# Kernel tuning notes

Measured on AMD Instinct MI355X. Metric: run time of the kernel, lower is better.

The kernel has to match this reference:

```python
import jax, jax.numpy as jnp
import numpy as np

SPATIAL_SHAPES = ((100, 100), (50, 50), (25, 25), (13, 13))
B, C, NH, NL, NP, DFF = 4, 256, 8, 4, 4, 1024
HD = C // NH
L = sum(h * w for h, w in SPATIAL_SHAPES)  # 13294


def _xavier(key, shape):
    s = (6.0 / (shape[0] + shape[1])) ** 0.5
    return jax.random.uniform(key, shape, jnp.float32, -s, s)


def setup_inputs():
    key = jax.random.key(0)
    ks = jax.random.split(key, 12)
    ss = jnp.array(SPATIAL_SHAPES, jnp.int32)
    lsi = jnp.concatenate([jnp.zeros((1,), jnp.int32), jnp.cumsum(ss[:, 0] * ss[:, 1])[:-1].astype(jnp.int32)])
    return {
        "query": jax.random.normal(ks[0], (B, L, C), jnp.float32),
        "query_pos": jax.random.normal(ks[1], (B, L, C), jnp.float32),
        "reference_points": jax.random.uniform(ks[2], (B, L, NL, 2), jnp.float32),
        "spatial_shapes": ss,
        "level_start_index": lsi,
        "v_W": _xavier(ks[3], (C, C)), "v_b": jnp.zeros((C,), jnp.float32),
        "off_W": 0.01 * jax.random.normal(ks[4], (C, NH * NL * NP * 2), jnp.float32),
        "off_b": 0.1 * jax.random.normal(ks[5], (NH * NL * NP * 2,), jnp.float32),
        "aw_W": 0.01 * jax.random.normal(ks[6], (C, NH * NL * NP), jnp.float32),
        "aw_b": jnp.zeros((NH * NL * NP,), jnp.float32),
        "out_W": _xavier(ks[7], (C, C)), "out_b": jnp.zeros((C,), jnp.float32),
        "ln1_g": jnp.ones((C,), jnp.float32), "ln1_b": jnp.zeros((C,), jnp.float32),
        "lin1_W": _xavier(ks[8], (C, DFF)), "lin1_b": jnp.zeros((DFF,), jnp.float32),
        "lin2_W": _xavier(ks[9], (DFF, C)), "lin2_b": jnp.zeros((C,), jnp.float32),
        "ln2_g": jnp.ones((C,), jnp.float32), "ln2_b": jnp.zeros((C,), jnp.float32),
    }


def _layer_norm(x, g, b):
    mu = x.mean(-1, keepdims=True)
    var = ((x - mu) ** 2).mean(-1, keepdims=True)
    return (x - mu) * jax.lax.rsqrt(var + 1e-5) * g + b


def _msda(q, value, reference_points, v_W, v_b, off_W, off_b, aw_W, aw_b, out_W, out_b):
    # value projection, split heads -> [B, NH, L, HD]
    v = (value @ v_W + v_b).reshape(B, L, NH, HD).transpose(0, 2, 1, 3)
    off = (q @ off_W + off_b).reshape(B, L, NH, NL, NP, 2)
    aw = jax.nn.softmax((q @ aw_W + aw_b).reshape(B, L, NH, NL * NP), axis=-1)
    aw = aw.reshape(B, L, NH, NL, NP).transpose(0, 2, 1, 3, 4)  # [B,NH,L,NL,NP]
    # offset normalizer is (W, H) per level, matching (x, y) coords
    norm = jnp.array([[w, h] for h, w in SPATIAL_SHAPES], q.dtype)
    loc = reference_points[:, :, None, :, None, :] + off / norm[None, None, None, :, None, :]
    loc = loc.transpose(0, 2, 1, 3, 4, 5)  # [B,NH,L,NL,NP,2]
    acc = jnp.zeros((B, NH, L, HD), q.dtype)
    start = 0
    for l, (H_, W_) in enumerate(SPATIAL_SHAPES):
        v_l = jax.lax.dynamic_slice_in_dim(v, start, H_ * W_, axis=2)  # [B,NH,HW,HD]
        # grid_sample(align_corners=False): pixel = loc*size - 0.5
        x = loc[:, :, :, l, :, 0] * W_ - 0.5  # [B,NH,L,NP]
        y = loc[:, :, :, l, :, 1] * H_ - 0.5
        x0 = jnp.floor(x); y0 = jnp.floor(y)
        lx = x - x0; ly = y - y0
        x0i = x0.astype(jnp.int32); y0i = y0.astype(jnp.int32)

        def corner(yi, xi, w):
            valid = (yi >= 0) & (yi < H_) & (xi >= 0) & (xi < W_)  # zero padding
            idx = jnp.clip(yi, 0, H_ - 1) * W_ + jnp.clip(xi, 0, W_ - 1)
            g = jnp.take_along_axis(v_l, idx.reshape(B, NH, L * NP, 1), axis=2)
            g = g.reshape(B, NH, L, NP, HD)
            return g * (w * valid)[..., None]

        s = (corner(y0i, x0i, (1 - ly) * (1 - lx))
             + corner(y0i, x0i + 1, (1 - ly) * lx)
             + corner(y0i + 1, x0i, ly * (1 - lx))
             + corner(y0i + 1, x0i + 1, ly * lx))  # [B,NH,L,NP,HD]
        acc = acc + (s * aw[:, :, :, l, :, None]).sum(3)
        start += H_ * W_
    out = acc.transpose(0, 2, 1, 3).reshape(B, L, C)
    return out @ out_W + out_b


def _forward(query, query_pos, reference_points, v_W, v_b, off_W, off_b, aw_W, aw_b,
             out_W, out_b, ln1_g, ln1_b, lin1_W, lin1_b, lin2_W, lin2_b, ln2_g, ln2_b):
    q = query + query_pos
    src2 = _msda(q, query, reference_points, v_W, v_b, off_W, off_b, aw_W, aw_b, out_W, out_b)
    x = _layer_norm(query + src2, ln1_g, ln1_b)
    ffn = jax.nn.relu(x @ lin1_W + lin1_b) @ lin2_W + lin2_b
    return _layer_norm(x + ffn, ln2_g, ln2_b)


def reference(query, query_pos, reference_points, spatial_shapes, level_start_index,
              v_W, v_b, off_W, off_b, aw_W, aw_b, out_W, out_b,
              ln1_g, ln1_b, lin1_W, lin1_b, lin2_W, lin2_b, ln2_g, ln2_b):
    # spatial_shapes / level_start_index are consistent with the static SPATIAL_SHAPES
    # constant (shapes must be static for reshapes under jit).
    return _forward(query, query_pos, reference_points, v_W, v_b, off_W, off_b, aw_W, aw_b,
                    out_W, out_b, ln1_g, ln1_b, lin1_W, lin1_b, lin2_W, lin2_b, ln2_g, ln2_b)
```

## Files before the change

### kernel.cpp

```cpp
#include <hip/hip_runtime.h>
#include <hip/hip_bf16.h>
#include <cstddef>

constexpr int Ll   = 13294;
constexpr int NROW = 4 * Ll;
constexpr int MP   = 53248;

typedef __bf16       bf8v __attribute__((ext_vector_type(8)));
typedef __bf16       bf2v __attribute__((ext_vector_type(2)));
typedef float        f4v  __attribute__((ext_vector_type(4)));
typedef unsigned int u4v  __attribute__((ext_vector_type(4)));

#if defined(__has_builtin)
#  if __has_builtin(__builtin_amdgcn_fdot2_f32_bf16)
#    define HAVE_DOT2_BF16 1
#  endif
#endif
#ifndef HAVE_DOT2_BF16
#  define HAVE_DOT2_BF16 0
#endif

__device__ __forceinline__ void xcd_remap(int& m0, int& n0)
{
    const int nwg  = gridDim.x * gridDim.y;
    const int flat = blockIdx.y * gridDim.x + blockIdx.x;
    const int w    = (flat & 7) * (nwg >> 3) + (flat >> 3);
    n0 = (w % gridDim.x) * 128;
    m0 = (w / gridDim.x) * 128;
}

template<bool RELU, bool OUTF, bool OUTB>
__device__ __forceinline__
void gemm_body(const __hip_bfloat16* __restrict__ A, const __hip_bfloat16* __restrict__ Bt,
               const float* __restrict__ bias, const float* __restrict__ bias2,
               float* __restrict__ Cf, __hip_bfloat16* __restrict__ Cb,
               int N, int K, int m0, int n0,
               __hip_bfloat16 (*As)[128 * 32], __hip_bfloat16 (*Bs)[128 * 32])
{
    const int tid  = threadIdx.x;
    const int wid  = tid >> 6;
    const int lane = tid & 63;
    const int wm = wid >> 1, wn = wid & 1;
    const int fr = lane & 15, fq = lane >> 4;
    const int sr = lane >> 2;
    const int sc = (lane & 3) * 8;

    f4v acc[4][4] = {};

    for (int k0 = 0; k0 < K; k0 += 64) {
        #pragma unroll
        for (int h = 0; h < 2; ++h) {
            #pragma unroll
            for (int i = 0; i < 2; ++i) {
                const int s = wid * 2 + i;
                const __hip_bfloat16* sa = A  + (size_t)(m0 + s * 16 + sr) * K + k0 + h * 32 + sc;
                const __hip_bfloat16* sb = Bt + (size_t)(n0 + s * 16 + sr) * K + k0 + h * 32 + sc;
                __builtin_amdgcn_global_load_lds(
                    (const __attribute__((address_space(1))) void*)sa,
                    (__attribute__((address_space(3))) void*)&As[h][s * 512], 16, 0, 0);
                __builtin_amdgcn_global_load_lds(
                    (const __attribute__((address_space(1))) void*)sb,
                    (__attribute__((address_space(3))) void*)&Bs[h][s * 512], 16, 0, 0);
            }
        }
        __syncthreads();

        #pragma unroll
        for (int h = 0; h < 2; ++h) {
            bf8v a[4], b[4];
            #pragma unroll
            for (int r = 0; r < 4; ++r) {
                a[r] = __builtin_bit_cast(bf8v, *(const u4v*)&As[h][(wm * 64 + r * 16 + fr) * 32 + fq * 8]);
                b[r] = __builtin_bit_cast(bf8v, *(const u4v*)&Bs[h][(wn * 64 + r * 16 + fr) * 32 + fq * 8]);
            }
            #pragma unroll
            for (int nr = 0; nr < 4; ++nr)
                #pragma unroll
                for (int mr = 0; mr < 4; ++mr)
                    acc[nr][mr] = __builtin_amdgcn_mfma_f32_16x16x32_bf16(b[nr], a[mr], acc[nr][mr], 0, 0, 0);
        }
        __syncthreads();
    }

    #pragma unroll
    for (int nr = 0; nr < 4; ++nr) {
        const int colbase = n0 + wn * 64 + nr * 16 + fq * 4;
        const float* bp = (bias2 != nullptr && colbase >= 256) ? (bias2 - 256) : bias;
        const float4 b4 = *(const float4*)&bp[colbase];
        #pragma unroll
        for (int mr = 0; mr < 4; ++mr) {
            const int row = m0 + wm * 64 + mr * 16 + fr;
            f4v v = acc[nr][mr];
            v[0] += b4.x; v[1] += b4.y; v[2] += b4.z; v[3] += b4.w;
            if (RELU) {
                v[0] = fmaxf(v[0], 0.f); v[1] = fmaxf(v[1], 0.f);
                v[2] = fmaxf(v[2], 0.f); v[3] = fmaxf(v[3], 0.f);
            }
            if (OUTF)
                *(float4*)&Cf[(size_t)row * N + colbase] = make_float4(v[0], v[1], v[2], v[3]);
            if (OUTB) {
                union { ushort4 u; __hip_bfloat16 h[4]; } pk;
                pk.h[0] = __float2bfloat16(v[0]); pk.h[1] = __float2bfloat16(v[1]);
                pk.h[2] = __float2bfloat16(v[2]); pk.h[3] = __float2bfloat16(v[3]);
                *(ushort4*)&Cb[(size_t)row * N + colbase] = pk.u;
            }
        }
    }
}

template<bool RELU, bool OUTF, bool OUTB>
__global__ __launch_bounds__(256)
void gemm_mfma(const __hip_bfloat16* __restrict__ A, const __hip_bfloat16* __restrict__ Bt,
               const float* __restrict__ bias, const float* __restrict__ bias2,
               float* __restrict__ Cf, __hip_bfloat16* __restrict__ Cb,
               int M, int N, int K)
{
    __shared__ __hip_bfloat16 As[2][128 * 32];
    __shared__ __hip_bfloat16 Bs[2][128 * 32];
    int m0, n0;
    xcd_remap(m0, n0);
    gemm_body<RELU, OUTF, OUTB>(A, Bt, bias, bias2, Cf, Cb, N, K, m0, n0, As, Bs);
}

__global__ __launch_bounds__(256)
void gemm_proj_pair(const __hip_bfloat16* __restrict__ qb, const __hip_bfloat16* __restrict__ qpb,
                    const __hip_bfloat16* __restrict__ vWt, const __hip_bfloat16* __restrict__ catWt,
                    const float* __restrict__ v_b, const float* __restrict__ off_b,
                    const float* __restrict__ aw_b,
                    __hip_bfloat16* __restrict__ vbuf, __hip_bfloat16* __restrict__ catb)
{
    __shared__ __hip_bfloat16 As[2][128 * 32];
    __shared__ __hip_bfloat16 Bs[2][128 * 32];
    const int nwg  = 2080;
    const int flat = blockIdx.x;
    const int w    = (flat & 7) * (nwg >> 3) + (flat >> 3);
    const int n    = w % 5, m = w / 5;
    if (n < 2)
        gemm_body<false, false, true>(qb, vWt, v_b, nullptr,
                                      nullptr, vbuf, 256, 256, m * 128, n * 128, As, Bs);
    else
        gemm_body<false, false, true>(qpb, catWt, off_b, aw_b,
                                      nullptr, catb, 384, 256, m * 128, (n - 2) * 128, As, Bs);
}

template<bool STOREB, bool RESB>
__global__ __launch_bounds__(256)
void gemm_ln(const __hip_bfloat16* __restrict__ A, const __hip_bfloat16* __restrict__ Bt,
             const float* __restrict__ bias,
             const float* __restrict__ resF, const __hip_bfloat16* __restrict__ resB,
             int Mres,
             const float* __restrict__ g, const float* __restrict__ be,
             float* __restrict__ outF, int MstoreF,
             __hip_bfloat16* __restrict__ outB,
             int K)
{
    __shared__ __hip_bfloat16 As[2][64 * 32];
    __shared__ __hip_bfloat16 Bs[2][256 * 32];
    __shared__ float red[2][64][2];
    const int tid  = threadIdx.x;
    const int wid  = tid >> 6;
    const int lane = tid & 63;
    const int m0 = blockIdx.x * 64;
    const int wm = wid >> 1, wn = wid & 1;
    const int fr = lane & 15, fq = lane >> 4;
    const int sr = lane >> 2;
    const int sc = (lane & 3) * 8;

    f4v acc[8][2] = {};

    for (int k0 = 0; k0 < K; k0 += 64) {
        #pragma unroll
        for (int h = 0; h < 2; ++h) {
            {
                const __hip_bfloat16* sa = A + (size_t)(m0 + wid * 16 + sr) * K + k0 + h * 32 + sc;
                __builtin_amdgcn_global_load_lds(
                    (const __attribute__((address_space(1))) void*)sa,
                    (__attribute__((address_space(3))) void*)&As[h][wid * 512], 16, 0, 0);
            }
            #pragma unroll
            for (int i = 0; i < 4; ++i) {
                const int s = wid * 4 + i;
                const __hip_bfloat16* sb = Bt + (size_t)(s * 16 + sr) * K + k0 + h * 32 + sc;
                __builtin_amdgcn_global_load_lds(
                    (const __attribute__((address_space(1))) void*)sb,
                    (__attribute__((address_space(3))) void*)&Bs[h][s * 512], 16, 0, 0);
            }
        }
        __syncthreads();

        #pragma unroll
        for (int h = 0; h < 2; ++h) {
            bf8v a[2], b[8];
            #pragma unroll
            for (int r = 0; r < 2; ++r)
                a[r] = __builtin_bit_cast(bf8v, *(const u4v*)&As[h][(wm * 32 + r * 16 + fr) * 32 + fq * 8]);
            #pragma unroll
            for (int r = 0; r < 8; ++r)
                b[r] = __builtin_bit_cast(bf8v, *(const u4v*)&Bs[h][(wn * 128 + r * 16 + fr) * 32 + fq * 8]);
            #pragma unroll
            for (int nr = 0; nr < 8; ++nr)
                #pragma unroll
                for (int mr = 0; mr < 2; ++mr)
                    acc[nr][mr] = __builtin_amdgcn_mfma_f32_16x16x32_bf16(b[nr], a[mr], acc[nr][mr], 0, 0, 0);
        }
        __syncthreads();
    }

    float s2[2] = {}, q2[2] = {};
    #pragma unroll
    for (int nr = 0; nr < 8; ++nr) {
        const int colbase = wn * 128 + nr * 16 + fq * 4;
        const float4 b4 = *(const float4*)&bias[colbase];
        #pragma unroll
        for (int mr = 0; mr < 2; ++mr) {
            const int row = m0 + wm * 32 + mr * 16 + fr;
            f4v x = acc[nr][mr];
            x[0] += b4.x; x[1] += b4.y; x[2] += b4.z; x[3] += b4.w;
            if (RESB) {
                const ushort4 r4 = *(const ushort4*)&resB[(size_t)row * 256 + colbase];
                x[0] += __builtin_bit_cast(float, (unsigned)r4.x << 16);
                x[1] += __builtin_bit_cast(float, (unsigned)r4.y << 16);
                x[2] += __builtin_bit_cast(float, (unsigned)r4.z << 16);
                x[3] += __builtin_bit_cast(float, (unsigned)r4.w << 16);
            } else if (row < Mres) {
                const float4 r4 = *(const float4*)&resF[(size_t)row * 256 + colbase];
                x[0] += r4.x; x[1] += r4.y; x[2] += r4.z; x[3] += r4.w;
            }
            acc[nr][mr] = x;
            s2[mr] += x[0] + x[1] + x[2] + x[3];
            q2[mr] += x[0]*x[0] + x[1]*x[1] + x[2]*x[2] + x[3]*x[3];
        }
    }
    #pragma unroll
    for (int mr = 0; mr < 2; ++mr) {
        s2[mr] += __shfl_xor(s2[mr], 16, 64);
        q2[mr] += __shfl_xor(q2[mr], 16, 64);
        s2[mr] += __shfl_xor(s2[mr], 32, 64);
        q2[mr] += __shfl_xor(q2[mr], 32, 64);
    }
    if (fq == 0) {
        #pragma unroll
        for (int mr = 0; mr < 2; ++mr) {
            red[wn][wm * 32 + mr * 16 + fr][0] = s2[mr];
            red[wn][wm * 32 + mr * 16 + fr][1] = q2[mr];
        }
    }
    __syncthreads();
    float mean[2], rinv[2];
    #pragma unroll
    for (int mr = 0; mr < 2; ++mr) {
        const int r = wm * 32 + mr * 16 + fr;
        const float ss = red[0][r][0] + red[1][r][0];
        const float qq = red[0][r][1] + red[1][r][1];
        mean[mr] = ss * (1.f / 256.f);
        const float var = qq * (1.f / 256.f) - mean[mr] * mean[mr];
        rinv[mr] = rsqrtf(var + 1e-5f);
    }
    #pragma unroll
    for (int nr = 0; nr < 8; ++nr) {
        const int colbase = wn * 128 + nr * 16 + fq * 4;
        const float4 g4 = *(const float4*)&g[colbase];
        const float4 e4 = *(const float4*)&be[colbase];
        #pragma unroll
        for (int mr = 0; mr < 2; ++mr) {
            const int row = m0 + wm * 32 + mr * 16 + fr;
            const f4v x = acc[nr][mr];
            float y0 = (x[0] - mean[mr]) * rinv[mr] * g4.x + e4.x;
            float y1 = (x[1] - mean[mr]) * rinv[mr] * g4.y + e4.y;
            float y2 = (x[2] - mean[mr]) * rinv[mr] * g4.z + e4.z;
            float y3 = (x[3] - mean[mr]) * rinv[mr] * g4.w + e4.w;
            if (row < MstoreF)
                *(float4*)&outF[(size_t)row * 256 + colbase] = make_float4(y0, y1, y2, y3);
            if (STOREB) {
                union { ushort4 u; __hip_bfloat16 h[4]; } pk;
                pk.h[0] = __float2bfloat16(y0); pk.h[1] = __float2bfloat16(y1);
                pk.h[2] = __float2bfloat16(y2); pk.h[3] = __float2bfloat16(y3);
                *(ushort4*)&outB[(size_t)row * 256 + colbase] = pk.u;
            }
        }
    }
}

__global__ __launch_bounds__(256)
void prep_all(const float* __restrict__ vW, const float* __restrict__ offW,
              const float* __restrict__ awW, const float* __restrict__ outW,
              const float* __restrict__ w1, const float* __restrict__ w2,
              __hip_bfloat16* __restrict__ vWt, __hip_bfloat16* __restrict__ catWt,
              __hip_bfloat16* __restrict__ outWt, __hip_bfloat16* __restrict__ w1t,
              __hip_bfloat16* __restrict__ w2t,
              const float* __restrict__ q, const float* __restrict__ qp,
              __hip_bfloat16* __restrict__ qb, __hip_bfloat16* __restrict__ qpb)
{
    if (blockIdx.x < 2944) {
        int i = blockIdx.x * 256 + threadIdx.x;
        if (i < 65536) { const int n = i >> 8, k = i & 255;
            vWt[i] = __float2bfloat16(vW[(size_t)k * 256 + n]); return; }
        i -= 65536;
        if (i < 98304) { const int n = i >> 8, k = i & 255;
            catWt[i] = __float2bfloat16(n < 256 ? offW[(size_t)k * 256 + n]
                                                : awW[(size_t)k * 128 + n - 256]); return; }
        i -= 98304;
        if (i < 65536) { const int n = i >> 8, k = i & 255;
            outWt[i] = __float2bfloat16(outW[(size_t)k * 256 + n]); return; }
        i -= 65536;
        if (i < 262144) { const int n = i >> 8, k = i & 255;
            w1t[i] = __float2bfloat16(w1[(size_t)k * 1024 + n]); return; }
        i -= 262144;
        { const int n = i >> 10, k = i & 1023;
            w2t[i] = __float2bfloat16(w2[(size_t)k * 256 + n]); }
        return;
    }
    const int i   = (blockIdx.x - 2944) * 256 + threadIdx.x;
    const int row = i >> 5;
    union { u4v u; __hip_bfloat16 h[8]; } p1, p2;
    if (row >= NROW) {
        u4v z = {0u, 0u, 0u, 0u};
        p1.u = z; p2.u = z;
    } else {
        const size_t e = (size_t)i * 8;
        float4 x0 = *(const float4*)&q[e];
        float4 x1 = *(const float4*)&q[e + 4];
        float4 y0 = *(const float4*)&qp[e];
        float4 y1 = *(const float4*)&qp[e + 4];
        p1.h[0] = __float2bfloat16(x0.x); p1.h[1] = __float2bfloat16(x0.y);
        p1.h[2] = __float2bfloat16(x0.z); p1.h[3] = __float2bfloat16(x0.w);
        p1.h[4] = __float2bfloat16(x1.x); p1.h[5] = __float2bfloat16(x1.y);
        p1.h[6] = __float2bfloat16(x1.z); p1.h[7] = __float2bfloat16(x1.w);
        p2.h[0] = __float2bfloat16(x0.x + y0.x); p2.h[1] = __float2bfloat16(x0.y + y0.y);
        p2.h[2] = __float2bfloat16(x0.z + y0.z); p2.h[3] = __float2bfloat16(x0.w + y0.w);
        p2.h[4] = __float2bfloat16(x1.x + y1.x); p2.h[5] = __float2bfloat16(x1.y + y1.y);
        p2.h[6] = __float2bfloat16(x1.z + y1.z); p2.h[7] = __float2bfloat16(x1.w + y1.w);
    }
    *(u4v*)&qb[(size_t)i * 8]  = p1.u;
    *(u4v*)&qpb[(size_t)i * 8] = p2.u;
}

__device__ __forceinline__ float blo(unsigned u) { return __builtin_bit_cast(float, u << 16); }
__device__ __forceinline__ float bhi(unsigned u) { return __builtin_bit_cast(float, u & 0xffff0000u); }

__global__ __launch_bounds__(256)
void msda_sample5(const __hip_bfloat16* __restrict__ v, const __hip_bfloat16* __restrict__ cat,
                  const float* __restrict__ refp, __hip_bfloat16* __restrict__ accO)
{
    __shared__ int      sIdx[1024][4];
    __shared__ unsigned sWpk[1024][2];
    int blk;
    {
        const int nwg  = gridDim.x;
        const int q    = nwg >> 3;
        const int r    = nwg & 7;
        const int xcd  = blockIdx.x & 7;
        const int off  = blockIdx.x >> 3;
        blk = (xcd < r ? xcd * (q + 1) : r * (q + 1) + (xcd - r) * q) + off;
    }
    const int row0 = blk * 8;
    const int tid  = threadIdx.x;

    #pragma unroll
    for (int it = 0; it < 4; ++it) {
        const int item = it * 256 + tid;
        const int p = item & 15, h = (item >> 4) & 7, r = item >> 7;
        const int row = row0 + r;
        const int lvl = p >> 2;
        const float logit = __bfloat162float(cat[(size_t)row * 384 + 256 + h * 16 + p]);
        float mx = logit;
        #pragma unroll
        for (int o = 1; o < 16; o <<= 1) mx = fmaxf(mx, __shfl_xor(mx, o, 64));
        const float e = __expf(logit - mx);
        float s = e;
        #pragma unroll
        for (int o = 1; o < 16; o <<= 1) s += __shfl_xor(s, o, 64);
        const float aw = e / s;

        const int Hs_[4] = {100, 50, 25, 13};
        const int Ss[4]  = {0, 10000, 12500, 13125};
        const int   Wl = Hs_[lvl];
        const float Wf = (float)Wl;
        const float ox = __bfloat162float(cat[(size_t)row * 384 + h * 32 + p * 2 + 0]);
        const float oy = __bfloat162float(cat[(size_t)row * 384 + h * 32 + p * 2 + 1]);
        const float rx = refp[(size_t)row * 8 + lvl * 2 + 0];
        const float ry = refp[(size_t)row * 8 + lvl * 2 + 1];
        const float x = (rx + ox / Wf) * Wf - 0.5f;
        const float y = (ry + oy / Wf) * Wf - 0.5f;
        const float x0f = floorf(x), y0f = floorf(y);
        const float lx = x - x0f, ly = y - y0f;
        const int x0 = (int)x0f, y0 = (int)y0f;
        const int b = row / Ll;
        const int vbase = b * Ll + Ss[lvl];
        int ixr[4]; unsigned short wb[4];
        #pragma unroll
        for (int c = 0; c < 4; ++c) {
            const int cy = c >> 1, cx = c & 1;
            const int yi = y0 + cy, xi = x0 + cx;
            const bool ok = (yi >= 0) & (yi < Wl) & (xi >= 0) & (xi < Wl);
            const int yc = min(max(yi, 0), Wl - 1);
            const int xc = min(max(xi, 0), Wl - 1);
            const float wt = (cy ? ly : 1.f - ly) * (cx ? lx : 1.f - lx);
            ixr[c] = (vbase + yc * Wl + xc) * 512;
            const __hip_bfloat16 hw = __float2bfloat16(ok ? aw * wt : 0.f);
            wb[c] = __builtin_bit_cast(unsigned short, hw);
        }
        const int item2 = (item & ~15) | ((item & 15) ^ h);
        *(int4*)&sIdx[item2][0] = make_int4(ixr[0], ixr[1], ixr[2], ixr[3]);
        sWpk[item2][0] = (unsigned)wb[0] | ((unsigned)wb[1] << 16);
        sWpk[item2][1] = (unsigned)wb[2] | ((unsigned)wb[3] << 16);
    }
    __syncthreads();

    const int r   = tid >> 5;
    const int h   = (tid >> 2) & 7;
    const int oct = tid & 3;
    const int row = row0 + r;
    const char* vB = (const char*)v + (h * 32 + oct * 8) * 2;
    const int ibase = r * 128 + h * 16;
    float acc[8] = {};
    #pragma unroll
    for (int i = 0; i < 16; ++i) {
        const int idx = ibase + (i ^ h);
        const int4  ix = *(const int4*)&sIdx[idx][0];
        const uint2 wp = *(const uint2*)&sWpk[idx][0];
        u4v u0 = *(const u4v*)(vB + (unsigned)ix.x);
        u4v u1 = *(const u4v*)(vB + (unsigned)ix.y);
        u4v u2 = *(const u4v*)(vB + (unsigned)ix.z);
        u4v u3 = *(const u4v*)(vB + (unsigned)ix.w);
#if HAVE_DOT2_BF16
        const bf2v w01 = __builtin_bit_cast(bf2v, wp.x);
        const bf2v w23 = __builtin_bit_cast(bf2v, wp.y);
        #pragma unroll
        for (int q = 0; q < 4; ++q) {
            const unsigned lo01 = __builtin_amdgcn_perm(u1[q], u0[q], 0x05040100u);
            const unsigned hi01 = __builtin_amdgcn_perm(u1[q], u0[q], 0x07060302u);
            const unsigned lo23 = __builtin_amdgcn_perm(u3[q], u2[q], 0x05040100u);
            const unsigned hi23 = __builtin_amdgcn_perm(u3[q], u2[q], 0x07060302u);
            acc[2*q]   = __builtin_amdgcn_fdot2_f32_bf16(__builtin_bit_cast(bf2v, lo01), w01, acc[2*q],   false);
            acc[2*q]   = __builtin_amdgcn_fdot2_f32_bf16(__builtin_bit_cast(bf2v, lo23), w23, acc[2*q],   false);
            acc[2*q+1] = __builtin_amdgcn_fdot2_f32_bf16(__builtin_bit_cast(bf2v, hi01), w01, acc[2*q+1], false);
            acc[2*q+1] = __builtin_amdgcn_fdot2_f32_bf16(__builtin_bit_cast(bf2v, hi23), w23, acc[2*q+1], false);
        }
#else
        const float w0 = blo(wp.x), w1 = bhi(wp.x);
        const float w2 = blo(wp.y), w3 = bhi(wp.y);
        #pragma unroll
        for (int q = 0; q < 4; ++q) {
            acc[2*q]   = fmaf(w0, blo(u0[q]), acc[2*q]);
            acc[2*q+1] = fmaf(w0, bhi(u0[q]), acc[2*q+1]);
            acc[2*q]   = fmaf(w1, blo(u1[q]), acc[2*q]);
            acc[2*q+1] = fmaf(w1, bhi(u1[q]), acc[2*q+1]);
            acc[2*q]   = fmaf(w2, blo(u2[q]), acc[2*q]);
            acc[2*q+1] = fmaf(w2, bhi(u2[q]), acc[2*q+1]);
            acc[2*q]   = fmaf(w3, blo(u3[q]), acc[2*q]);
            acc[2*q+1] = fmaf(w3, bhi(u3[q]), acc[2*q+1]);
        }
#endif
    }
    union { u4v u; __hip_bfloat16 hh[8]; } pk;
    #pragma unroll
    for (int q = 0; q < 8; ++q) pk.hh[q] = __float2bfloat16(acc[q]);
    *(u4v*)&accO[(size_t)row * 256 + h * 32 + oct * 8] = pk.u;
}

extern "C" void kernel_launch(void* const* d_in, const int* in_sizes, int n_in,
                              void* d_out, int out_size, void* d_ws, size_t ws_size,
                              hipStream_t stream)
{
    (void)in_sizes; (void)n_in; (void)out_size; (void)ws_size;
    const float* query = (const float*)d_in[0];
    const float* qpos  = (const float*)d_in[1];
    const float* refp  = (const float*)d_in[2];
    const float* v_W   = (const float*)d_in[5];
    const float* v_b   = (const float*)d_in[6];
    const float* off_W = (const float*)d_in[7];
    const float* off_b = (const float*)d_in[8];
    const float* aw_W  = (const float*)d_in[9];
    const float* aw_b  = (const float*)d_in[10];
    const float* out_W = (const float*)d_in[11];
    const float* out_b = (const float*)d_in[12];
    const float* ln1g  = (const float*)d_in[13];
    const float* ln1b  = (const float*)d_in[14];
    const float* w1    = (const float*)d_in[15];
    const float* b1    = (const float*)d_in[16];
    const float* w2    = (const float*)d_in[17];
    const float* b2    = (const float*)d_in[18];
    const float* ln2g  = (const float*)d_in[19];
    const float* ln2b  = (const float*)d_in[20];
    float* out = (float*)d_out;

    char* ws = (char*)d_ws;
    constexpr size_t HALF_B = (size_t)MP * 256 * 2;
    constexpr size_t HBUF_B = (size_t)MP * 1024 * 2;
    __hip_bfloat16* hbuf = (__hip_bfloat16*)ws;
    __hip_bfloat16* qb   = (__hip_bfloat16*)ws;
    __hip_bfloat16* qpb  = (__hip_bfloat16*)(ws + HALF_B);
    __hip_bfloat16* catb = (__hip_bfloat16*)(ws + 2 * HALF_B);
    __hip_bfloat16* vbuf = (__hip_bfloat16*)(ws + HBUF_B);
    __hip_bfloat16* accb = qpb;
    __hip_bfloat16* xb   = vbuf;
    char* wsw = ws + HBUF_B + HALF_B;
    __hip_bfloat16* vWt   = (__hip_bfloat16*)(wsw);
    __hip_bfloat16* catWt = (__hip_bfloat16*)(wsw + 131072);
    __hip_bfloat16* outWt = (__hip_bfloat16*)(wsw + 327680);
    __hip_bfloat16* w1t   = (__hip_bfloat16*)(wsw + 458752);
    __hip_bfloat16* w2t   = (__hip_bfloat16*)(wsw + 983040);

    dim3 blk(256);

    prep_all<<<2944 + MP / 8, blk, 0, stream>>>(
        v_W, off_W, aw_W, out_W, w1, w2, vWt, catWt, outWt, w1t, w2t,
        query, qpos, qb, qpb);

    gemm_proj_pair<<<2080, blk, 0, stream>>>(
        qb, qpb, vWt, catWt, v_b, off_b, aw_b, vbuf, catb);

    msda_sample5<<<NROW / 8, blk, 0, stream>>>(vbuf, catb, refp, accb);

    gemm_ln<true, true><<<MP / 64, blk, 0, stream>>>(
        accb, outWt, out_b, nullptr, qb, MP, ln1g, ln1b,
        nullptr, 0, xb, 256);

    gemm_mfma<true, false, true><<<dim3(8, MP / 128), blk, 0, stream>>>(
        xb, w1t, b1, nullptr, nullptr, hbuf, MP, 1024, 256);

    gemm_ln<false, true><<<MP / 64, blk, 0, stream>>>(
        hbuf, w2t, b2, nullptr, xb, MP, ln2g, ln2b,
        out, NROW, nullptr, 1024);
}
```

Baseline: 331.7 us.

## Double-buffer LDS staging in GEMM kernels to overlap loads with MFMA

Reworks both GEMM main loops so the two 32-wide K halves act as ping-pong LDS buffers. The next half is issued via global_load_lds while MFMAs run on the current one, with an explicit waitcnt+barrier between stages. MFMA sections are also wrapped in s_setprio to favour the compute wave. The aim is to hide global-to-LDS latency that the old load-all-then-compute scheme left exposed. In exchange, barriers per 64-K step go from two to two-plus-prologue, and correctness now depends on getting the buffer-reuse ordering right.

```diff
diff --git a/kernel.cpp b/kernel.cpp
--- a/kernel.cpp
+++ b/kernel.cpp
@@ -20,6 +20,10 @@
 #  define HAVE_DOT2_BF16 0
 #endif
 
+#define WAIT_BARRIER() do { \
+    asm volatile("s_waitcnt vmcnt(0) lgkmcnt(0)" ::: "memory"); \
+    __builtin_amdgcn_s_barrier(); } while (0)
+
 __device__ __forceinline__ void xcd_remap(int& m0, int& n0)
 {
     const int nwg  = gridDim.x * gridDim.y;
@@ -27,6 +31,13 @@
     const int w    = (flat & 7) * (nwg >> 3) + (flat >> 3);
     n0 = (w % gridDim.x) * 128;
     m0 = (w / gridDim.x) * 128;
+}
+
+__device__ __forceinline__ void gload16(const __hip_bfloat16* src, __hip_bfloat16* dst)
+{
+    __builtin_amdgcn_global_load_lds(
+        (const __attribute__((address_space(1))) void*)src,
+        (__attribute__((address_space(3))) void*)dst, 16, 0, 0);
 }
 
 template<bool RELU, bool OUTF, bool OUTB>
@@ -47,39 +58,39 @@
 
     f4v acc[4][4] = {};
 
+    auto stage = [&](int buf, int kk) {
+        #pragma unroll
+        for (int i = 0; i < 2; ++i) {
+            const int s = wid * 2 + i;
+            gload16(A  + (size_t)(m0 + s * 16 + sr) * K + kk + sc, &As[buf][s * 512]);
+            gload16(Bt + (size_t)(n0 + s * 16 + sr) * K + kk + sc, &Bs[buf][s * 512]);
+        }
+    };
+    auto compute = [&](int buf) {
+        bf8v a[4], b[4];
+        #pragma unroll
+        for (int r = 0; r < 4; ++r) {
+            a[r] = __builtin_bit_cast(bf8v, *(const u4v*)&As[buf][(wm * 64 + r * 16 + fr) * 32 + fq * 8]);
+            b[r] = __builtin_bit_cast(bf8v, *(const u4v*)&Bs[buf][(wn * 64 + r * 16 + fr) * 32 + fq * 8]);
+        }
+        __builtin_amdgcn_s_setprio(1);
+        #pragma unroll
+        for (int nr = 0; nr < 4; ++nr)
+            #pragma unroll
+            for (int mr = 0; mr < 4; ++mr)
+                acc[nr][mr] = __builtin_amdgcn_mfma_f32_16x16x32_bf16(b[nr], a[mr], acc[nr][mr], 0, 0, 0);
+        __builtin_amdgcn_s_setprio(0);
+    };
+
+    stage(0, 0);
+    WAIT_BARRIER();
     for (int k0 = 0; k0 < K; k0 += 64) {
-        #pragma unroll
-        for (int h = 0; h < 2; ++h) {
-            #pragma unroll
-            for (int i = 0; i < 2; ++i) {
-                const int s = wid * 2 + i;
-                const __hip_bfloat16* sa = A  + (size_t)(m0 + s * 16 + sr) * K + k0 + h * 32 + sc;
-                const __hip_bfloat16* sb = Bt + (size_t)(n0 + s * 16 + sr) * K + k0 + h * 32 + sc;
-                __builtin_amdgcn_global_load_lds(
-                    (const __attribute__((address_space(1))) void*)sa,
-                    (__attribute__((address_space(3))) void*)&As[h][s * 512], 16, 0, 0);
-                __builtin_amdgcn_global_load_lds(
-                    (const __attribute__((address_space(1))) void*)sb,
-                    (__attribute__((address_space(3))) void*)&Bs[h][s * 512], 16, 0, 0);
-            }
-        }
-        __syncthreads();
-
-        #pragma unroll
-        for (int h = 0; h < 2; ++h) {
-            bf8v a[4], b[4];
-            #pragma unroll
-            for (int r = 0; r < 4; ++r) {
-                a[r] = __builtin_bit_cast(bf8v, *(const u4v*)&As[h][(wm * 64 + r * 16 + fr) * 32 + fq * 8]);
-                b[r] = __builtin_bit_cast(bf8v, *(const u4v*)&Bs[h][(wn * 64 + r * 16 + fr) * 32 + fq * 8]);
-            }
-            #pragma unroll
-            for (int nr = 0; nr < 4; ++nr)
-                #pragma unroll
-                for (int mr = 0; mr < 4; ++mr)
-                    acc[nr][mr] = __builtin_amdgcn_mfma_f32_16x16x32_bf16(b[nr], a[mr], acc[nr][mr], 0, 0, 0);
-        }
-        __syncthreads();
+        stage(1, k0 + 32);
+        compute(0);
+        WAIT_BARRIER();
+        if (k0 + 64 < K) stage(0, k0 + 64);
+        compute(1);
+        WAIT_BARRIER();
     }
 
     #pragma unroll
@@ -168,42 +179,40 @@
 
     f4v acc[8][2] = {};
 
+    auto stage = [&](int buf, int kk) {
+        gload16(A + (size_t)(m0 + wid * 16 + sr) * K + kk + sc, &As[buf][wid * 512]);
+        #pragma unroll
+        for (int i = 0; i < 4; ++i) {
+            const int s = wid * 4 + i;
+            gload16(Bt + (size_t)(s * 16 + sr) * K + kk + sc, &Bs[buf][s * 512]);
+        }
+    };
+    auto compute = [&](int buf) {
+        bf8v a[2], b[8];
+        #pragma unroll
+        for (int r = 0; r < 2; ++r)
+            a[r] = __builtin_bit_cast(bf8v, *(const u4v*)&As[buf][(wm * 32 + r * 16 + fr) * 32 + fq * 8]);
+        #pragma unroll
+        for (int r = 0; r < 8; ++r)
+            b[r] = __builtin_bit_cast(bf8v, *(const u4v*)&Bs[buf][(wn * 128 + r * 16 + fr) * 32 + fq * 8]);
+        __builtin_amdgcn_s_setprio(1);
+        #pragma unroll
+        for (int nr = 0; nr < 8; ++nr)
+            #pragma unroll
+            for (int mr = 0; mr < 2; ++mr)
+                acc[nr][mr] = __builtin_amdgcn_mfma_f32_16x16x32_bf16(b[nr], a[mr], acc[nr][mr], 0, 0, 0);
+        __builtin_amdgcn_s_setprio(0);
+    };
+
+    stage(0, 0);
+    WAIT_BARRIER();
     for (int k0 = 0; k0 < K; k0 += 64) {
-        #pragma unroll
-        for (int h = 0; h < 2; ++h) {
-            {
-                const __hip_bfloat16* sa = A + (size_t)(m0 + wid * 16 + sr) * K + k0 + h * 32 + sc;
-                __builtin_amdgcn_global_load_lds(
-                    (const __attribute__((address_space(1))) void*)sa,
-                    (__attribute__((address_space(3))) void*)&As[h][wid * 512], 16, 0, 0);
-            }
-            #pragma unroll
-            for (int i = 0; i < 4; ++i) {
-                const int s = wid * 4 + i;
-                const __hip_bfloat16* sb = Bt + (size_t)(s * 16 + sr) * K + k0 + h * 32 + sc;
-                __builtin_amdgcn_global_load_lds(
-                    (const __attribute__((address_space(1))) void*)sb,
-                    (__attribute__((address_space(3))) void*)&Bs[h][s * 512], 16, 0, 0);
-            }
-        }
-        __syncthreads();
-
-        #pragma unroll
-        for (int h = 0; h < 2; ++h) {
-            bf8v a[2], b[8];
-            #pragma unroll
-            for (int r = 0; r < 2; ++r)
-                a[r] = __builtin_bit_cast(bf8v, *(const u4v*)&As[h][(wm * 32 + r * 16 + fr) * 32 + fq * 8]);
-            #pragma unroll
-            for (int r = 0; r < 8; ++r)
-                b[r] = __builtin_bit_cast(bf8v, *(const u4v*)&Bs[h][(wn * 128 + r * 16 + fr) * 32 + fq * 8]);
-            #pragma unroll
-            for (int nr = 0; nr < 8; ++nr)
-                #pragma unroll
-                for (int mr = 0; mr < 2; ++mr)
-                    acc[nr][mr] = __builtin_amdgcn_mfma_f32_16x16x32_bf16(b[nr], a[mr], acc[nr][mr], 0, 0, 0);
-        }
-        __syncthreads();
+        stage(1, k0 + 32);
+        compute(0);
+        WAIT_BARRIER();
+        if (k0 + 64 < K) stage(0, k0 + 64);
+        compute(1);
+        WAIT_BARRIER();
     }
 
     float s2[2] = {}, q2[2] = {};
```

New measurement: 331.0 us (median of 3 runs). Within noise of the previous version (-0.2%).
